# Performance work log

Hardware: AMD Instinct MI355X
Metric: run time of the kernel (lower is better)

Reference implementation:

```python
import jax, jax.numpy as jnp
import numpy as np

B, T, D = 2, 2048, 1024
H, DH, CTX = 16, 64, 2048
EPS = 1e-6

def setup_inputs() -> dict:
    key = jax.random.key(0)
    ks = jax.random.split(key, 8)
    s = lambda d: 1.0 / np.sqrt(d)
    return {
        'x':       jax.random.normal(ks[0], (B, T, D), jnp.float32),
        'w_norm1': jnp.ones((D,), jnp.float32),
        'w_qkv':   jax.random.normal(ks[1], (3 * D, D), jnp.float32) * s(D),
        'w_proj':  jax.random.normal(ks[2], (D, D), jnp.float32) * s(D),
        'w_norm2': jnp.ones((D,), jnp.float32),
        'w_gate':  jax.random.normal(ks[3], (4 * D, D), jnp.float32) * s(D),
        'w_up':    jax.random.normal(ks[4], (4 * D, D), jnp.float32) * s(D),
        'w_down':  jax.random.normal(ks[5], (D, 4 * D), jnp.float32) * s(4 * D),
        'step':    0,
    }

def _rmsnorm(x, w):
    return x * jax.lax.rsqrt(jnp.mean(x * x, axis=-1, keepdims=True) + EPS) * w

def reference(x, w_norm1, w_qkv, w_proj, w_norm2, w_gate, w_up, w_down, step):
    # Prefill path (kv_cache is None, step == 0): full causal attention over T tokens.
    b, t, d = x.shape
    scale = 1.0 / np.sqrt(DH)
    h = _rmsnorm(x, w_norm1)
    qkv = (h @ w_qkv.T).reshape(b, t, 3, H, DH).transpose(2, 0, 3, 1, 4)  # [3,B,H,T,Dh]
    q, k, v = qkv[0], qkv[1], qkv[2]
    att = jnp.einsum('bhqd,bhkd->bhqk', q, k) * scale           # [B,H,T,T]
    causal = jnp.tril(jnp.ones((t, t), bool))
    att = jnp.where(causal, att, jnp.float32(-jnp.inf))
    att = jax.nn.softmax(att, axis=-1)
    out = jnp.einsum('bhqk,bhkd->bhqd', att, v)                 # [B,H,T,Dh]
    out = out.transpose(0, 2, 1, 3).reshape(b, t, d)
    x = x + out @ w_proj.T
    h2 = _rmsnorm(x, w_norm2)
    x = x + (jax.nn.silu(h2 @ w_gate.T) * (h2 @ w_up.T)) @ w_down.T
    # Append-only KV cache, zero-padded to ctx length as in the torch module.
    k_cache = jnp.zeros((b, H, CTX, DH), x.dtype).at[:, :, :t].set(k)
    v_cache = jnp.zeros((b, H, CTX, DH), x.dtype).at[:, :, :t].set(v)
    return (x, k_cache, v_cache)
```

## Files before the change

### kernel.cpp

```cpp
#include <hip/hip_runtime.h>
#include <hip/hip_bf16.h>
#include <cstdint>
#include <cstddef>


using bf16x8 = __attribute__((ext_vector_type(8))) __bf16;
using f32x4  = __attribute__((ext_vector_type(4))) float;

#define VMCNT(n) asm volatile("s_waitcnt vmcnt(" #n ")" ::: "memory")
#define LGKM0()  do { asm volatile("s_waitcnt lgkmcnt(0)" ::: "memory"); \
                      __builtin_amdgcn_sched_barrier(0); } while (0)
#define BARF()   do { asm volatile("" ::: "memory"); __builtin_amdgcn_s_barrier(); \
                      asm volatile("" ::: "memory"); } while (0)

__device__ __forceinline__ short f2b(float f) {
  uint32_t u = __builtin_bit_cast(uint32_t, f);
  uint32_t r = (u + 0x7FFFu + ((u >> 16) & 1u)) >> 16;
  return (short)r;
}
__device__ __forceinline__ float b2f(short s) {
  uint32_t u = ((uint32_t)(uint16_t)s) << 16;
  return __builtin_bit_cast(float, u);
}
__device__ __forceinline__ uint32_t pack2(float a, float b) {
  return (__builtin_bit_cast(uint32_t, a) >> 16) |
         (__builtin_bit_cast(uint32_t, b) & 0xFFFF0000u);
}

__device__ __forceinline__ void gload16(const short* g, short* l) {
  __builtin_amdgcn_global_load_lds(
      (const __attribute__((address_space(1))) void*)g,
      (__attribute__((address_space(3))) void*)l, 16, 0, 0);
}

template<int ROWS>
__device__ __forceinline__ void stage_swz(const short* __restrict__ g, int ldg,
                                          short* lds, int tid) {
#pragma unroll
  for (int jj = 0; jj < ROWS / 32; ++jj) {
    int row = jj * 32 + (tid >> 3);
    int seg = tid & 7;
    gload16(g + (size_t)row * ldg + ((seg ^ (row & 7)) << 3),
            lds + row * 64 + (seg << 3));
  }
}

__device__ __forceinline__ void stage_round512(const short* __restrict__ g, int ldg,
                                               short* lds, int tid, int rbase) {
  int row = rbase + (tid >> 3);
  int seg = tid & 7;
  gload16(g + (size_t)row * ldg + ((seg ^ (row & 7)) << 3),
          lds + row * 64 + (seg << 3));
}

__device__ __forceinline__ bf16x8 frag64(const short* lds, int row, int seg) {
  return *(const bf16x8*)(lds + row * 64 + ((seg ^ (row & 7)) << 3));
}

__device__ __forceinline__ f32x4 mma16(bf16x8 a, bf16x8 b, f32x4 c) {
  return __builtin_amdgcn_mfma_f32_16x16x32_bf16(a, b, c, 0, 0, 0);
}

__global__ void k_cvt_all(const float* __restrict__ wqkv, short* __restrict__ oqkv,
                          const float* __restrict__ wproj, short* __restrict__ oproj,
                          const float* __restrict__ wgate, short* __restrict__ ogate,
                          const float* __restrict__ wup, short* __restrict__ oup,
                          const float* __restrict__ wdown, short* __restrict__ odown) {
  int bid = blockIdx.x;
  const float* src;
  short* dst;
  int off;
  if (bid < 3072)       { src = wqkv;  dst = oqkv;  off = bid; }
  else if (bid < 4096)  { src = wproj; dst = oproj; off = bid - 3072; }
  else if (bid < 8192)  { src = wgate; dst = ogate; off = bid - 4096; }
  else if (bid < 12288) { src = wup;   dst = oup;   off = bid - 8192; }
  else                  { src = wdown; dst = odown; off = bid - 12288; }
  int i = off * 256 + threadIdx.x;
  float4 v = ((const float4*)src)[i];
  ((short4*)dst)[i] = make_short4(f2b(v.x), f2b(v.y), f2b(v.z), f2b(v.w));
}

__global__ void k_rms(const float* __restrict__ x, const float* __restrict__ w,
                      short* __restrict__ out) {
  int row = blockIdx.x;
  int tid = threadIdx.x;
  float4 v = *(const float4*)(x + (size_t)row * 1024 + tid * 4);
  float ss = v.x * v.x + v.y * v.y + v.z * v.z + v.w * v.w;
#pragma unroll
  for (int o = 1; o < 64; o <<= 1) ss += __shfl_xor(ss, o);
  __shared__ float sred[4];
  int wid = tid >> 6, lane = tid & 63;
  if (lane == 0) sred[wid] = ss;
  __syncthreads();
  float tot = sred[0] + sred[1] + sred[2] + sred[3];
  float r = rsqrtf(tot * (1.0f / 1024.0f) + 1e-6f);
  float4 wv = *(const float4*)(w + tid * 4);
  short4 o = make_short4(f2b(v.x * r * wv.x), f2b(v.y * r * wv.y),
                         f2b(v.z * r * wv.z), f2b(v.w * r * wv.w));
  *(short4*)(out + (size_t)row * 1024 + tid * 4) = o;
}

__global__ __launch_bounds__(512) void k_qkv(
    const short* __restrict__ A, const short* __restrict__ W,
    short* __restrict__ q_b, short* __restrict__ k_b, short* __restrict__ vT_b,
    float* __restrict__ kc, float* __restrict__ vc) {
  const int K = 1024, nk = 16;
  __shared__ short As[2][128 * 64];
  __shared__ short Bq[2][128 * 64];
  __shared__ short Bk[2][128 * 64];
  __shared__ short Bv[2][128 * 64];
  int tid = threadIdx.x;
  int bid = blockIdx.x;
  int swz = (bid & 7) * 32 + (bid >> 3);
  int bx = swz & 7, by = swz >> 3;
  int m0 = by * 128, n0 = bx * 128;
  int w = tid >> 6, l = tid & 63;
  int wr = w >> 2, wc = w & 3;
  int lr = l & 15, lseg = l >> 4;
  f32x4 aq[4][2] = {}, ak[4][2] = {}, av[4][2] = {};
  const short* Ab = A + (size_t)m0 * K;
  const short* Qb = W + (size_t)n0 * K;
  const short* Kb = W + (size_t)(1024 + n0) * K;
  const short* Vb = W + (size_t)(2048 + n0) * K;

  stage_round512(Ab, K, &As[0][0], tid, 0);
  stage_round512(Ab, K, &As[0][0], tid, 64);
  stage_round512(Qb, K, &Bq[0][0], tid, 0);
  stage_round512(Qb, K, &Bq[0][0], tid, 64);
  stage_round512(Kb, K, &Bk[0][0], tid, 0);
  stage_round512(Kb, K, &Bk[0][0], tid, 64);
  stage_round512(Vb, K, &Bv[0][0], tid, 0);
  stage_round512(Vb, K, &Bv[0][0], tid, 64);
  stage_round512(Ab + 64, K, &As[1][0], tid, 0);
  stage_round512(Ab + 64, K, &As[1][0], tid, 64);

  bf16x8 a[4][2], b[2][2];
#pragma unroll 2
  for (int t = 0; t < nk; ++t) {
    short* Sa = &As[t & 1][0];
    short* Sq = &Bq[t & 1][0];
    short* Sk = &Bk[t & 1][0];
    short* Sv = &Bv[t & 1][0];
    short* SqN = &Bq[(t + 1) & 1][0];
    short* SkN = &Bk[(t + 1) & 1][0];
    short* SvN = &Bv[(t + 1) & 1][0];
    const short* Ag2 = Ab + (size_t)(t + 2) * 64;
    const short* Qg1 = Qb + (size_t)(t + 1) * 64;
    const short* Kg1 = Kb + (size_t)(t + 1) * 64;
    const short* Vg1 = Vb + (size_t)(t + 1) * 64;
    bool pf1 = (t + 1 < nk), pf2 = (t + 2 < nk);

    VMCNT(2);
    BARF();

#pragma unroll
    for (int i = 0; i < 4; ++i)
#pragma unroll
      for (int kk = 0; kk < 2; ++kk)
        a[i][kk] = frag64(Sa, wr * 64 + i * 16 + lr, kk * 4 + lseg);
#pragma unroll
    for (int j = 0; j < 2; ++j)
#pragma unroll
      for (int kk = 0; kk < 2; ++kk)
        b[j][kk] = frag64(Sq, wc * 32 + j * 16 + lr, kk * 4 + lseg);
    if (pf1) {
      stage_round512(Qg1, K, SqN, tid, 0);
      stage_round512(Qg1, K, SqN, tid, 64);
      stage_round512(Kg1, K, SkN, tid, 0);
      stage_round512(Kg1, K, SkN, tid, 64);
    }
    BARF();
    LGKM0();
    __builtin_amdgcn_s_setprio(1);
#pragma unroll
    for (int i = 0; i < 4; ++i)
#pragma unroll
      for (int j = 0; j < 2; ++j) {
        aq[i][j] = mma16(a[i][0], b[j][0], aq[i][j]);
        aq[i][j] = mma16(a[i][1], b[j][1], aq[i][j]);
      }
    __builtin_amdgcn_s_setprio(0);

#pragma unroll
    for (int j = 0; j < 2; ++j)
#pragma unroll
      for (int kk = 0; kk < 2; ++kk)
        b[j][kk] = frag64(Sk, wc * 32 + j * 16 + lr, kk * 4 + lseg);
    if (pf1) {
      stage_round512(Vg1, K, SvN, tid, 0);
      stage_round512(Vg1, K, SvN, tid, 64);
    }
    BARF();
    LGKM0();
    __builtin_amdgcn_s_setprio(1);
#pragma unroll
    for (int i = 0; i < 4; ++i)
#pragma unroll
      for (int j = 0; j < 2; ++j) {
        ak[i][j] = mma16(a[i][0], b[j][0], ak[i][j]);
        ak[i][j] = mma16(a[i][1], b[j][1], ak[i][j]);
      }
    __builtin_amdgcn_s_setprio(0);

#pragma unroll
    for (int j = 0; j < 2; ++j)
#pragma unroll
      for (int kk = 0; kk < 2; ++kk)
        b[j][kk] = frag64(Sv, wc * 32 + j * 16 + lr, kk * 4 + lseg);
    if (pf2) {
      stage_round512(Ag2, K, Sa, tid, 0);
      stage_round512(Ag2, K, Sa, tid, 64);
    }
    BARF();
    LGKM0();
    __builtin_amdgcn_s_setprio(1);
#pragma unroll
    for (int i = 0; i < 4; ++i)
#pragma unroll
      for (int j = 0; j < 2; ++j) {
        av[i][j] = mma16(a[i][0], b[j][0], av[i][j]);
        av[i][j] = mma16(a[i][1], b[j][1], av[i][j]);
      }
    __builtin_amdgcn_s_setprio(0);
  }

#pragma unroll
  for (int i = 0; i < 4; ++i) {
#pragma unroll
    for (int j = 0; j < 2; ++j) {
#pragma unroll
      for (int r = 0; r < 4; ++r) {
        int m = m0 + wr * 64 + i * 16 + lseg * 4 + r;
        int n = n0 + wc * 32 + j * 16 + lr;
        int hh = n >> 6, dh = n & 63;
        int b_ = m >> 11, tt = m & 2047;
        int bh = b_ * 16 + hh;
        size_t idx = ((size_t)bh * 2048 + tt) * 64 + dh;
        q_b[idx] = f2b(aq[i][j][r]);
        float fk = ak[i][j][r];
        k_b[idx] = f2b(fk);
        kc[idx] = fk;
        float fv = av[i][j][r];
        vT_b[((size_t)bh * 64 + dh) * 2048 + tt] = f2b(fv);
        vc[idx] = fv;
      }
    }
  }
}

__global__ __launch_bounds__(512) void k_mlp(
    const short* __restrict__ A, const short* __restrict__ Wg,
    const short* __restrict__ Wu, short* __restrict__ outb) {
  const int K = 1024, N = 4096, nk = 16;
  __shared__ short As[2][256 * 64];
  __shared__ short Bg[2][128 * 64];
  __shared__ short Bu[2][128 * 64];
  int tid = threadIdx.x;
  int nwg = gridDim.x, bid = blockIdx.x;
  int swz = (bid & 7) * (nwg >> 3) + (bid >> 3);
  int bx = swz & 31, by = swz >> 5;
  int m0 = by * 256, n0 = bx * 128;
  int w = tid >> 6, l = tid & 63;
  int wr = w >> 2, wc = w & 3;
  int lr = l & 15, lseg = l >> 4;
  f32x4 aG[2][4][2] = {}, aU[2][4][2] = {};
  const short* Ab = A + (size_t)m0 * K;
  const short* Gb = Wg + (size_t)n0 * K;
  const short* Ub = Wu + (size_t)n0 * K;

  stage_round512(Ab, K, &As[0][0], tid, 0);
  stage_round512(Ab, K, &As[0][0], tid, 64);
  stage_round512(Ab, K, &As[0][0], tid, 128);
  stage_round512(Ab, K, &As[0][0], tid, 192);
  stage_round512(Gb, K, &Bg[0][0], tid, 0);
  stage_round512(Gb, K, &Bg[0][0], tid, 64);
  stage_round512(Ub, K, &Bu[0][0], tid, 0);
  stage_round512(Ub, K, &Bu[0][0], tid, 64);
  stage_round512(Ab + 64, K, &As[1][0], tid, 0);
  stage_round512(Ab + 64, K, &As[1][0], tid, 64);
  stage_round512(Ab + 64, K, &As[1][0], tid, 128);
  stage_round512(Ab + 64, K, &As[1][0], tid, 192);

  bf16x8 a0[4][2], a1[4][2], bg[2][2], bu[2][2];
#pragma unroll 2
  for (int t = 0; t < nk; ++t) {
    short* Sa  = &As[t & 1][0];
    short* Sg  = &Bg[t & 1][0];
    short* Su  = &Bu[t & 1][0];
    short* SgN = &Bg[(t + 1) & 1][0];
    short* SuN = &Bu[(t + 1) & 1][0];
    const short* Ag2 = Ab + (size_t)(t + 2) * 64;
    const short* Gg1 = Gb + (size_t)(t + 1) * 64;
    const short* Ug1 = Ub + (size_t)(t + 1) * 64;
    bool pf1 = (t + 1 < nk), pf2 = (t + 2 < nk);

    VMCNT(4);
    BARF();

#pragma unroll
    for (int i = 0; i < 4; ++i)
#pragma unroll
      for (int kk = 0; kk < 2; ++kk)
        a0[i][kk] = frag64(Sa, wr * 128 + i * 16 + lr, kk * 4 + lseg);
#pragma unroll
    for (int j = 0; j < 2; ++j)
#pragma unroll
      for (int kk = 0; kk < 2; ++kk)
        bg[j][kk] = frag64(Sg, wc * 32 + j * 16 + lr, kk * 4 + lseg);
    if (pf1) {
      stage_round512(Gg1, K, SgN, tid, 0);
      stage_round512(Gg1, K, SgN, tid, 64);
      stage_round512(Ug1, K, SuN, tid, 0);
      stage_round512(Ug1, K, SuN, tid, 64);
    }
    BARF();
    LGKM0();
    __builtin_amdgcn_s_setprio(1);
#pragma unroll
    for (int i = 0; i < 4; ++i)
#pragma unroll
      for (int j = 0; j < 2; ++j) {
        aG[0][i][j] = mma16(a0[i][0], bg[j][0], aG[0][i][j]);
        aG[0][i][j] = mma16(a0[i][1], bg[j][1], aG[0][i][j]);
      }
    __builtin_amdgcn_s_setprio(0);

#pragma unroll
    for (int j = 0; j < 2; ++j)
#pragma unroll
      for (int kk = 0; kk < 2; ++kk)
        bu[j][kk] = frag64(Su, wc * 32 + j * 16 + lr, kk * 4 + lseg);
    if (pf2) {
      stage_round512(Ag2, K, Sa, tid, 0);
      stage_round512(Ag2, K, Sa, tid, 128);
    }
    BARF();
    LGKM0();
    __builtin_amdgcn_s_setprio(1);
#pragma unroll
    for (int i = 0; i < 4; ++i)
#pragma unroll
      for (int j = 0; j < 2; ++j) {
        aU[0][i][j] = mma16(a0[i][0], bu[j][0], aU[0][i][j]);
        aU[0][i][j] = mma16(a0[i][1], bu[j][1], aU[0][i][j]);
      }
    __builtin_amdgcn_s_setprio(0);

#pragma unroll
    for (int i = 0; i < 4; ++i)
#pragma unroll
      for (int kk = 0; kk < 2; ++kk)
        a1[i][kk] = frag64(Sa, wr * 128 + 64 + i * 16 + lr, kk * 4 + lseg);
    BARF();
    LGKM0();
    __builtin_amdgcn_s_setprio(1);
#pragma unroll
    for (int i = 0; i < 4; ++i)
#pragma unroll
      for (int j = 0; j < 2; ++j) {
        aG[1][i][j] = mma16(a1[i][0], bg[j][0], aG[1][i][j]);
        aG[1][i][j] = mma16(a1[i][1], bg[j][1], aG[1][i][j]);
      }
    __builtin_amdgcn_s_setprio(0);

    if (pf2) {
      stage_round512(Ag2, K, Sa, tid, 64);
      stage_round512(Ag2, K, Sa, tid, 192);
    }
    BARF();
    __builtin_amdgcn_s_setprio(1);
#pragma unroll
    for (int i = 0; i < 4; ++i)
#pragma unroll
      for (int j = 0; j < 2; ++j) {
        aU[1][i][j] = mma16(a1[i][0], bu[j][0], aU[1][i][j]);
        aU[1][i][j] = mma16(a1[i][1], bu[j][1], aU[1][i][j]);
      }
    __builtin_amdgcn_s_setprio(0);
  }

#pragma unroll
  for (int qm = 0; qm < 2; ++qm) {
#pragma unroll
    for (int i = 0; i < 4; ++i) {
#pragma unroll
      for (int j = 0; j < 2; ++j) {
#pragma unroll
        for (int r = 0; r < 4; ++r) {
          int m = m0 + wr * 128 + qm * 64 + i * 16 + (l >> 4) * 4 + r;
          int n = n0 + wc * 32 + j * 16 + lr;
          float g = aG[qm][i][j][r];
          float u = aU[qm][i][j][r];
          float s = g / (1.0f + __expf(-g));
          outb[(size_t)m * N + n] = f2b(s * u);
        }
      }
    }
  }
}

__global__ __launch_bounds__(256, 2) void k_gemm_skinny(
    const short* __restrict__ A, const short* __restrict__ Bw,
    int M, int N, int K, int gx,
    const float* __restrict__ res, float* __restrict__ outf) {
  __shared__ short As[3][128 * 64];
  __shared__ short Bs[3][64 * 64];
  int tid = threadIdx.x;
  int nwg = gridDim.x, bid = blockIdx.x;
  int swz = (bid & 7) * (nwg >> 3) + (bid >> 3);
  int bx = swz % gx, by = swz / gx;
  int m0 = by * 128, n0 = bx * 64;
  int w = tid >> 6, l = tid & 63;
  int wr = w >> 1, wc = w & 1;
  int lr = l & 15, lseg = l >> 4;
  f32x4 acc[4][2] = {};
  int nk = K >> 6;
  const short* Ab = A + (size_t)m0 * K;
  const short* Bb = Bw + (size_t)n0 * K;

  stage_swz<128>(Ab, K, &As[0][0], tid);
  stage_swz<64>(Bb, K, &Bs[0][0], tid);
  stage_swz<128>(Ab + 64, K, &As[1][0], tid);
  stage_swz<64>(Bb + 64, K, &Bs[1][0], tid);

#pragma unroll 1
  for (int u = 0; u < nk; ++u) {
    VMCNT(6);
    BARF();
    if (u + 2 < nk) {
      int sl = (u + 2) % 3;
      stage_swz<128>(Ab + (u + 2) * 64, K, &As[sl][0], tid);
      stage_swz<64>(Bb + (u + 2) * 64, K, &Bs[sl][0], tid);
    }
    const short* Asl = &As[u % 3][0];
    const short* Bsl = &Bs[u % 3][0];
    bf16x8 ar[4][2], br[2][2];
#pragma unroll
    for (int i = 0; i < 4; ++i)
#pragma unroll
      for (int kk = 0; kk < 2; ++kk)
        ar[i][kk] = frag64(Asl, wr * 64 + i * 16 + lr, kk * 4 + lseg);
#pragma unroll
    for (int j = 0; j < 2; ++j)
#pragma unroll
      for (int kk = 0; kk < 2; ++kk)
        br[j][kk] = frag64(Bsl, wc * 32 + j * 16 + lr, kk * 4 + lseg);
    LGKM0();
    __builtin_amdgcn_s_setprio(1);
#pragma unroll
    for (int i = 0; i < 4; ++i)
#pragma unroll
      for (int j = 0; j < 2; ++j) {
        acc[i][j] = mma16(ar[i][0], br[j][0], acc[i][j]);
        acc[i][j] = mma16(ar[i][1], br[j][1], acc[i][j]);
      }
    __builtin_amdgcn_s_setprio(0);
  }

#pragma unroll
  for (int i = 0; i < 4; ++i) {
#pragma unroll
    for (int j = 0; j < 2; ++j) {
#pragma unroll
      for (int r = 0; r < 4; ++r) {
        int m = m0 + wr * 64 + i * 16 + (l >> 4) * 4 + r;
        int n = n0 + wc * 32 + j * 16 + lr;
        outf[(size_t)m * N + n] = acc[i][j][r] + res[(size_t)m * N + n];
      }
    }
  }
}

template<int NC>
__device__ __forceinline__ void attn_tile(
    const short* __restrict__ Ksl, const short* __restrict__ Vsl,
    short* __restrict__ pw,
    const bf16x8 (&qf)[2][2], f32x4 (&acc)[2][4],
    float (&mrow)[2], float (&dden)[2],
    int kv0, int qb0, int qb1, bool band0, bool band1,
    int lr, int g) {
  bf16x8 kf[4][2], vb[2][4];
#pragma unroll
  for (int i = 0; i < 4; ++i)
#pragma unroll
    for (int kk = 0; kk < 2; ++kk)
      kf[i][kk] = frag64(Ksl, i * 16 + lr, kk * 4 + g);
#pragma unroll
  for (int kk = 0; kk < 2; ++kk)
#pragma unroll
    for (int jf = 0; jf < 4; ++jf)
      vb[kk][jf] = frag64(Vsl, jf * 16 + lr, kk * 4 + g);

  f32x4 st[NC][4];
#pragma unroll
  for (int c = 0; c < NC; ++c) {
    int cc = (NC == 2) ? c : 1;
#pragma unroll
    for (int i = 0; i < 4; ++i) {
      f32x4 z = {};
      z = mma16(kf[i][0], qf[cc][0], z);
      z = mma16(kf[i][1], qf[cc][1], z);
      st[c][i] = z;
    }
  }

  const float SC = 0.125f * 1.44269504f;
  float p[NC][16], pm[NC], corr[NC];
#pragma unroll
  for (int c = 0; c < NC; ++c) {
    int cc = (NC == 2) ? c : 1;
    bool band = (cc == 0) ? band0 : band1;
    int qgc = ((cc == 0) ? qb0 : qb1) + lr;
    float m_ = -INFINITY;
#pragma unroll
    for (int i = 0; i < 4; ++i)
#pragma unroll
      for (int r = 0; r < 4; ++r) {
        float v = st[c][i][r] * SC;
        if (band) {
          int key = kv0 + i * 16 + g * 4 + r;
          if (key > qgc) v = -INFINITY;
        }
        p[c][i * 4 + r] = v;
        m_ = fmaxf(m_, v);
      }
    pm[c] = m_;
  }
#pragma unroll
  for (int c = 0; c < NC; ++c) pm[c] = fmaxf(pm[c], __shfl_xor(pm[c], 16));
#pragma unroll
  for (int c = 0; c < NC; ++c) pm[c] = fmaxf(pm[c], __shfl_xor(pm[c], 32));
  float dsum[NC];
#pragma unroll
  for (int c = 0; c < NC; ++c) {
    int cc = (NC == 2) ? c : 1;
    float nm = fmaxf(mrow[cc], pm[c]);
    corr[c] = exp2f(mrow[cc] - nm);
    mrow[cc] = nm;
    float ds_ = 0.0f;
#pragma unroll
    for (int kx = 0; kx < 16; ++kx) {
      float pv = exp2f(p[c][kx] - nm);
      p[c][kx] = pv;
      ds_ += pv;
    }
    dsum[c] = ds_;
  }
#pragma unroll
  for (int c = 0; c < NC; ++c) dsum[c] += __shfl_xor(dsum[c], 16);
#pragma unroll
  for (int c = 0; c < NC; ++c) dsum[c] += __shfl_xor(dsum[c], 32);
#pragma unroll
  for (int c = 0; c < NC; ++c) {
    int cc = (NC == 2) ? c : 1;
    dden[cc] = dden[cc] * corr[c] + dsum[c];
  }

#pragma unroll
  for (int c = 0; c < NC; ++c) {
    int cc = (NC == 2) ? c : 1;
#pragma unroll
    for (int r = 0; r < 4; ++r) {
      float cr = __shfl(corr[c], g * 4 + r);
#pragma unroll
      for (int jf = 0; jf < 4; ++jf) acc[cc][jf][r] *= cr;
    }
    int prow = cc * 16 + lr;
#pragma unroll
    for (int i = 0; i < 4; ++i) {
      uint2 pk;
      pk.x = pack2(p[c][i * 4 + 0], p[c][i * 4 + 1]);
      pk.y = pack2(p[c][i * 4 + 2], p[c][i * 4 + 3]);
      int seg = (i * 2 + (g >> 1)) ^ (prow & 7);
      *(uint2*)(pw + prow * 64 + seg * 8 + (g & 1) * 4) = pk;
    }
  }

#pragma unroll
  for (int c = 0; c < NC; ++c) {
    int cc = (NC == 2) ? c : 1;
    int prow = cc * 16 + lr;
#pragma unroll
    for (int kk = 0; kk < 2; ++kk) {
      bf16x8 pa = *(const bf16x8*)(pw + prow * 64 + (((kk * 4 + g) ^ (prow & 7)) << 3));
#pragma unroll
      for (int jf = 0; jf < 4; ++jf)
        acc[cc][jf] = mma16(pa, vb[kk][jf], acc[cc][jf]);
    }
  }
}

__global__ __launch_bounds__(256, 2) void k_attn(const short* __restrict__ q_b,
                                                 const short* __restrict__ k_b,
                                                 const short* __restrict__ vT_b,
                                                 short* __restrict__ o_b) {
  __shared__ short Ks[3][64 * 64];
  __shared__ short VTs[3][64 * 64];
  __shared__ short Ps[4][32 * 64];
  int tid = threadIdx.x;
  int w = tid >> 6, l = tid & 63;
  int lr = l & 15, g = l >> 4;
  int ib = blockIdx.x, bh = blockIdx.y;
  int qlo = ib, qhi = 31 - ib;
  int qb0 = qlo * 64 + w * 16;
  int qb1 = qhi * 64 + w * 16;

  bf16x8 qf[2][2];
  const short* Qg = q_b + (size_t)bh * 2048 * 64;
#pragma unroll
  for (int kk = 0; kk < 2; ++kk) {
    qf[0][kk] = *(const bf16x8*)(Qg + (size_t)(qb0 + lr) * 64 + kk * 32 + g * 8);
    qf[1][kk] = *(const bf16x8*)(Qg + (size_t)(qb1 + lr) * 64 + kk * 32 + g * 8);
  }

  f32x4 acc[2][4] = {};
  float mrow[2] = {-INFINITY, -INFINITY};
  float dden[2] = {0.0f, 0.0f};
  int nt = qhi + 1;
  const short* Kg = k_b + (size_t)bh * 2048 * 64;
  const short* Vg = vT_b + (size_t)bh * 64 * 2048;
  short* pw = &Ps[w][0];

  stage_swz<64>(Kg, 64, &Ks[0][0], tid);
  stage_swz<64>(Vg, 2048, &VTs[0][0], tid);
  stage_swz<64>(Kg + 64 * 64, 64, &Ks[1][0], tid);
  stage_swz<64>(Vg + 64, 2048, &VTs[1][0], tid);

#pragma unroll 1
  for (int kt = 0; kt <= qlo; ++kt) {
    VMCNT(4);
    BARF();
    if (kt + 2 < nt) {
      int sl = (kt + 2) % 3;
      stage_swz<64>(Kg + (size_t)(kt + 2) * 64 * 64, 64, &Ks[sl][0], tid);
      stage_swz<64>(Vg + (kt + 2) * 64, 2048, &VTs[sl][0], tid);
    }
    int s = kt % 3;
    attn_tile<2>(&Ks[s][0], &VTs[s][0], pw, qf, acc, mrow, dden,
                 kt * 64, qb0, qb1, kt == qlo, false, lr, g);
  }
#pragma unroll 1
  for (int kt = qlo + 1; kt < nt; ++kt) {
    VMCNT(4);
    BARF();
    if (kt + 2 < nt) {
      int sl = (kt + 2) % 3;
      stage_swz<64>(Kg + (size_t)(kt + 2) * 64 * 64, 64, &Ks[sl][0], tid);
      stage_swz<64>(Vg + (kt + 2) * 64, 2048, &VTs[sl][0], tid);
    }
    int s = kt % 3;
    attn_tile<1>(&Ks[s][0], &VTs[s][0], pw, qf, acc, mrow, dden,
                 kt * 64, qb0, qb1, false, kt == qhi, lr, g);
  }

  int hh = bh & 15, b_ = bh >> 4;
#pragma unroll
  for (int c = 0; c < 2; ++c) {
    int qbc = (c == 0) ? qb0 : qb1;
#pragma unroll
    for (int r = 0; r < 4; ++r) {
      float dq = __shfl(dden[c], g * 4 + r);
      float inv = 1.0f / dq;
      int mg = qbc + g * 4 + r;
      size_t rowoff = ((size_t)b_ * 2048 + mg) * 1024 + hh * 64;
#pragma unroll
      for (int jf = 0; jf < 4; ++jf)
        o_b[rowoff + jf * 16 + lr] = f2b(acc[c][jf][r] * inv);
    }
  }
}

extern "C" void kernel_launch(void* const* d_in, const int* in_sizes, int n_in,
                              void* d_out, int out_size, void* d_ws, size_t ws_size,
                              hipStream_t stream) {
  const float* x     = (const float*)d_in[0];
  const float* wn1   = (const float*)d_in[1];
  const float* wqkv  = (const float*)d_in[2];
  const float* wproj = (const float*)d_in[3];
  const float* wn2   = (const float*)d_in[4];
  const float* wgate = (const float*)d_in[5];
  const float* wup   = (const float*)d_in[6];
  const float* wdown = (const float*)d_in[7];
  float* out = (float*)d_out;
  char* ws = (char*)d_ws;

  short* wqkv_b  = (short*)(ws + 0);
  short* wproj_b = (short*)(ws + 6291456);
  short* wgate_b = (short*)(ws + 8388608);
  short* wup_b   = (short*)(ws + 16777216);
  short* wdown_b = (short*)(ws + 25165824);
  short* h_b     = (short*)(ws + 33554432);
  short* q_b     = (short*)(ws + 41943040);
  short* k_b     = (short*)(ws + 50331648);
  short* vT_b    = (short*)(ws + 58720256);
  short* ao_b    = (short*)(ws + 67108864);
  short* act_b   = q_b;
  float* x1 = out;
  float* kc = out + 4194304;
  float* vc = out + 8388608;

  k_cvt_all<<<16384, 256, 0, stream>>>(wqkv, wqkv_b, wproj, wproj_b,
                                       wgate, wgate_b, wup, wup_b, wdown, wdown_b);

  k_rms<<<4096, 256, 0, stream>>>(x, wn1, h_b);

  k_qkv<<<256, 512, 0, stream>>>(h_b, wqkv_b, q_b, k_b, vT_b, kc, vc);

  k_attn<<<dim3(16, 32), 256, 0, stream>>>(q_b, k_b, vT_b, ao_b);

  k_gemm_skinny<<<512, 256, 0, stream>>>(ao_b, wproj_b, 4096, 1024, 1024, 16,
                                         x, x1);

  k_rms<<<4096, 256, 0, stream>>>(x1, wn2, h_b);

  k_mlp<<<512, 512, 0, stream>>>(h_b, wgate_b, wup_b, act_b);

  k_gemm_skinny<<<512, 256, 0, stream>>>(act_b, wdown_b, 4096, 1024, 4096, 16,
                                         x1, out);
}
```

Before: 279.6 us.

## Halve GEMM grids to one wave of workgroups with larger per-block tiles

The MLP gate/up kernel now launches 256 workgroups, and each one loops over two adjacent 128-column output tiles, restaging the A tile for each half. The skinny GEMM used for the projection and down projection grows its M tile from 128 to 256 rows, doubles the accumulators and drops from a three-stage to a two-stage buffer with a full vmcnt wait. The aim is a single full wave of blocks on the 256 CUs to avoid a tail wave, plus more reuse of each B tile. In exchange there is less latency hiding (vmcnt 0, double buffering), more register and LDS pressure, and the MLP's two halves run serially inside each block.

```diff
diff --git a/kernel.cpp b/kernel.cpp
--- a/kernel.cpp
+++ b/kernel.cpp
@@ -256,146 +256,152 @@
   __shared__ short Bg[2][128 * 64];
   __shared__ short Bu[2][128 * 64];
   int tid = threadIdx.x;
-  int nwg = gridDim.x, bid = blockIdx.x;
-  int swz = (bid & 7) * (nwg >> 3) + (bid >> 3);
-  int bx = swz & 31, by = swz >> 5;
-  int m0 = by * 256, n0 = bx * 128;
+  int bid = blockIdx.x;
+  int swz = (bid & 7) * 32 + (bid >> 3);
+  int bxp = swz & 15, by = swz >> 4;
+  int m0 = by * 256;
   int w = tid >> 6, l = tid & 63;
   int wr = w >> 2, wc = w & 3;
   int lr = l & 15, lseg = l >> 4;
-  f32x4 aG[2][4][2] = {}, aU[2][4][2] = {};
   const short* Ab = A + (size_t)m0 * K;
-  const short* Gb = Wg + (size_t)n0 * K;
-  const short* Ub = Wu + (size_t)n0 * K;
-
-  stage_round512(Ab, K, &As[0][0], tid, 0);
-  stage_round512(Ab, K, &As[0][0], tid, 64);
-  stage_round512(Ab, K, &As[0][0], tid, 128);
-  stage_round512(Ab, K, &As[0][0], tid, 192);
-  stage_round512(Gb, K, &Bg[0][0], tid, 0);
-  stage_round512(Gb, K, &Bg[0][0], tid, 64);
-  stage_round512(Ub, K, &Bu[0][0], tid, 0);
-  stage_round512(Ub, K, &Bu[0][0], tid, 64);
-  stage_round512(Ab + 64, K, &As[1][0], tid, 0);
-  stage_round512(Ab + 64, K, &As[1][0], tid, 64);
-  stage_round512(Ab + 64, K, &As[1][0], tid, 128);
-  stage_round512(Ab + 64, K, &As[1][0], tid, 192);
-
-  bf16x8 a0[4][2], a1[4][2], bg[2][2], bu[2][2];
+
+#pragma unroll 1
+  for (int hf = 0; hf < 2; ++hf) {
+    int n0 = (bxp * 2 + hf) * 128;
+    const short* Gb = Wg + (size_t)n0 * K;
+    const short* Ub = Wu + (size_t)n0 * K;
+    f32x4 aG[2][4][2] = {}, aU[2][4][2] = {};
+
+    stage_round512(Ab, K, &As[0][0], tid, 0);
+    stage_round512(Ab, K, &As[0][0], tid, 64);
+    stage_round512(Ab, K, &As[0][0], tid, 128);
+    stage_round512(Ab, K, &As[0][0], tid, 192);
+    stage_round512(Gb, K, &Bg[0][0], tid, 0);
+    stage_round512(Gb, K, &Bg[0][0], tid, 64);
+    stage_round512(Ub, K, &Bu[0][0], tid, 0);
+    stage_round512(Ub, K, &Bu[0][0], tid, 64);
+    stage_round512(Ab + 64, K, &As[1][0], tid, 0);
+    stage_round512(Ab + 64, K, &As[1][0], tid, 64);
+    stage_round512(Ab + 64, K, &As[1][0], tid, 128);
+    stage_round512(Ab + 64, K, &As[1][0], tid, 192);
+
+    bf16x8 a0[4][2], a1[4][2], bg[2][2], bu[2][2];
 #pragma unroll 2
-  for (int t = 0; t < nk; ++t) {
-    short* Sa  = &As[t & 1][0];
-    short* Sg  = &Bg[t & 1][0];
-    short* Su  = &Bu[t & 1][0];
-    short* SgN = &Bg[(t + 1) & 1][0];
-    short* SuN = &Bu[(t + 1) & 1][0];
-    const short* Ag2 = Ab + (size_t)(t + 2) * 64;
-    const short* Gg1 = Gb + (size_t)(t + 1) * 64;
-    const short* Ug1 = Ub + (size_t)(t + 1) * 64;
-    bool pf1 = (t + 1 < nk), pf2 = (t + 2 < nk);
-
-    VMCNT(4);
+    for (int t = 0; t < nk; ++t) {
+      short* Sa  = &As[t & 1][0];
+      short* Sg  = &Bg[t & 1][0];
+      short* Su  = &Bu[t & 1][0];
+      short* SgN = &Bg[(t + 1) & 1][0];
+      short* SuN = &Bu[(t + 1) & 1][0];
+      const short* Ag2 = Ab + (size_t)(t + 2) * 64;
+      const short* Gg1 = Gb + (size_t)(t + 1) * 64;
+      const short* Ug1 = Ub + (size_t)(t + 1) * 64;
+      bool pf1 = (t + 1 < nk), pf2 = (t + 2 < nk);
+
+      VMCNT(4);
+      BARF();
+
+#pragma unroll
+      for (int i = 0; i < 4; ++i)
+#pragma unroll
+        for (int kk = 0; kk < 2; ++kk)
+          a0[i][kk] = frag64(Sa, wr * 128 + i * 16 + lr, kk * 4 + lseg);
+#pragma unroll
+      for (int j = 0; j < 2; ++j)
+#pragma unroll
+        for (int kk = 0; kk < 2; ++kk)
+          bg[j][kk] = frag64(Sg, wc * 32 + j * 16 + lr, kk * 4 + lseg);
+      if (pf1) {
+        stage_round512(Gg1, K, SgN, tid, 0);
+        stage_round512(Gg1, K, SgN, tid, 64);
+        stage_round512(Ug1, K, SuN, tid, 0);
+        stage_round512(Ug1, K, SuN, tid, 64);
+      }
+      BARF();
+      LGKM0();
+      __builtin_amdgcn_s_setprio(1);
+#pragma unroll
+      for (int i = 0; i < 4; ++i)
+#pragma unroll
+        for (int j = 0; j < 2; ++j) {
+          aG[0][i][j] = mma16(a0[i][0], bg[j][0], aG[0][i][j]);
+          aG[0][i][j] = mma16(a0[i][1], bg[j][1], aG[0][i][j]);
+        }
+      __builtin_amdgcn_s_setprio(0);
+
+#pragma unroll
+      for (int j = 0; j < 2; ++j)
+#pragma unroll
+        for (int kk = 0; kk < 2; ++kk)
+          bu[j][kk] = frag64(Su, wc * 32 + j * 16 + lr, kk * 4 + lseg);
+      if (pf2) {
+        stage_round512(Ag2, K, Sa, tid, 0);
+        stage_round512(Ag2, K, Sa, tid, 128);
+      }
+      BARF();
+      LGKM0();
+      __builtin_amdgcn_s_setprio(1);
+#pragma unroll
+      for (int i = 0; i < 4; ++i)
+#pragma unroll
+        for (int j = 0; j < 2; ++j) {
+          aU[0][i][j] = mma16(a0[i][0], bu[j][0], aU[0][i][j]);
+          aU[0][i][j] = mma16(a0[i][1], bu[j][1], aU[0][i][j]);
+        }
+      __builtin_amdgcn_s_setprio(0);
+
+#pragma unroll
+      for (int i = 0; i < 4; ++i)
+#pragma unroll
+        for (int kk = 0; kk < 2; ++kk)
+          a1[i][kk] = frag64(Sa, wr * 128 + 64 + i * 16 + lr, kk * 4 + lseg);
+      BARF();
+      LGKM0();
+      __builtin_amdgcn_s_setprio(1);
+#pragma unroll
+      for (int i = 0; i < 4; ++i)
+#pragma unroll
+        for (int j = 0; j < 2; ++j) {
+          aG[1][i][j] = mma16(a1[i][0], bg[j][0], aG[1][i][j]);
+          aG[1][i][j] = mma16(a1[i][1], bg[j][1], aG[1][i][j]);
+        }
+      __builtin_amdgcn_s_setprio(0);
+
+      if (pf2) {
+        stage_round512(Ag2, K, Sa, tid, 64);
+        stage_round512(Ag2, K, Sa, tid, 192);
+      }
+      BARF();
+      __builtin_amdgcn_s_setprio(1);
+#pragma unroll
+      for (int i = 0; i < 4; ++i)
+#pragma unroll
+        for (int j = 0; j < 2; ++j) {
+          aU[1][i][j] = mma16(a1[i][0], bu[j][0], aU[1][i][j]);
+          aU[1][i][j] = mma16(a1[i][1], bu[j][1], aU[1][i][j]);
+        }
+      __builtin_amdgcn_s_setprio(0);
+    }
+
+#pragma unroll
+    for (int qm = 0; qm < 2; ++qm) {
+#pragma unroll
+      for (int i = 0; i < 4; ++i) {
+#pragma unroll
+        for (int j = 0; j < 2; ++j) {
+#pragma unroll
+          for (int r = 0; r < 4; ++r) {
+            int m = m0 + wr * 128 + qm * 64 + i * 16 + lseg * 4 + r;
+            int n = n0 + wc * 32 + j * 16 + lr;
+            float g = aG[qm][i][j][r];
+            float u = aU[qm][i][j][r];
+            float s = g / (1.0f + __expf(-g));
+            outb[(size_t)m * N + n] = f2b(s * u);
+          }
+        }
+      }
+    }
     BARF();
-
-#pragma unroll
-    for (int i = 0; i < 4; ++i)
-#pragma unroll
-      for (int kk = 0; kk < 2; ++kk)
-        a0[i][kk] = frag64(Sa, wr * 128 + i * 16 + lr, kk * 4 + lseg);
-#pragma unroll
-    for (int j = 0; j < 2; ++j)
-#pragma unroll
-      for (int kk = 0; kk < 2; ++kk)
-        bg[j][kk] = frag64(Sg, wc * 32 + j * 16 + lr, kk * 4 + lseg);
-    if (pf1) {
-      stage_round512(Gg1, K, SgN, tid, 0);
-      stage_round512(Gg1, K, SgN, tid, 64);
-      stage_round512(Ug1, K, SuN, tid, 0);
-      stage_round512(Ug1, K, SuN, tid, 64);
-    }
-    BARF();
-    LGKM0();
-    __builtin_amdgcn_s_setprio(1);
-#pragma unroll
-    for (int i = 0; i < 4; ++i)
-#pragma unroll
-      for (int j = 0; j < 2; ++j) {
-        aG[0][i][j] = mma16(a0[i][0], bg[j][0], aG[0][i][j]);
-        aG[0][i][j] = mma16(a0[i][1], bg[j][1], aG[0][i][j]);
-      }
-    __builtin_amdgcn_s_setprio(0);
-
-#pragma unroll
-    for (int j = 0; j < 2; ++j)
-#pragma unroll
-      for (int kk = 0; kk < 2; ++kk)
-        bu[j][kk] = frag64(Su, wc * 32 + j * 16 + lr, kk * 4 + lseg);
-    if (pf2) {
-      stage_round512(Ag2, K, Sa, tid, 0);
-      stage_round512(Ag2, K, Sa, tid, 128);
-    }
-    BARF();
-    LGKM0();
-    __builtin_amdgcn_s_setprio(1);
-#pragma unroll
-    for (int i = 0; i < 4; ++i)
-#pragma unroll
-      for (int j = 0; j < 2; ++j) {
-        aU[0][i][j] = mma16(a0[i][0], bu[j][0], aU[0][i][j]);
-        aU[0][i][j] = mma16(a0[i][1], bu[j][1], aU[0][i][j]);
-      }
-    __builtin_amdgcn_s_setprio(0);
-
-#pragma unroll
-    for (int i = 0; i < 4; ++i)
-#pragma unroll
-      for (int kk = 0; kk < 2; ++kk)
-        a1[i][kk] = frag64(Sa, wr * 128 + 64 + i * 16 + lr, kk * 4 + lseg);
-    BARF();
-    LGKM0();
-    __builtin_amdgcn_s_setprio(1);
-#pragma unroll
-    for (int i = 0; i < 4; ++i)
-#pragma unroll
-      for (int j = 0; j < 2; ++j) {
-        aG[1][i][j] = mma16(a1[i][0], bg[j][0], aG[1][i][j]);
-        aG[1][i][j] = mma16(a1[i][1], bg[j][1], aG[1][i][j]);
-      }
-    __builtin_amdgcn_s_setprio(0);
-
-    if (pf2) {
-      stage_round512(Ag2, K, Sa, tid, 64);
-      stage_round512(Ag2, K, Sa, tid, 192);
-    }
-    BARF();
-    __builtin_amdgcn_s_setprio(1);
-#pragma unroll
-    for (int i = 0; i < 4; ++i)
-#pragma unroll
-      for (int j = 0; j < 2; ++j) {
-        aU[1][i][j] = mma16(a1[i][0], bu[j][0], aU[1][i][j]);
-        aU[1][i][j] = mma16(a1[i][1], bu[j][1], aU[1][i][j]);
-      }
-    __builtin_amdgcn_s_setprio(0);
-  }
-
-#pragma unroll
-  for (int qm = 0; qm < 2; ++qm) {
-#pragma unroll
-    for (int i = 0; i < 4; ++i) {
-#pragma unroll
-      for (int j = 0; j < 2; ++j) {
-#pragma unroll
-        for (int r = 0; r < 4; ++r) {
-          int m = m0 + wr * 128 + qm * 64 + i * 16 + (l >> 4) * 4 + r;
-          int n = n0 + wc * 32 + j * 16 + lr;
-          float g = aG[qm][i][j][r];
-          float u = aU[qm][i][j][r];
-          float s = g / (1.0f + __expf(-g));
-          outb[(size_t)m * N + n] = f2b(s * u);
-        }
-      }
-    }
   }
 }
 
@@ -403,67 +409,80 @@
     const short* __restrict__ A, const short* __restrict__ Bw,
     int M, int N, int K, int gx,
     const float* __restrict__ res, float* __restrict__ outf) {
-  __shared__ short As[3][128 * 64];
-  __shared__ short Bs[3][64 * 64];
+  __shared__ short As[2][256 * 64];
+  __shared__ short Bs[2][64 * 64];
   int tid = threadIdx.x;
   int nwg = gridDim.x, bid = blockIdx.x;
   int swz = (bid & 7) * (nwg >> 3) + (bid >> 3);
   int bx = swz % gx, by = swz / gx;
-  int m0 = by * 128, n0 = bx * 64;
+  int m0 = by * 256, n0 = bx * 64;
   int w = tid >> 6, l = tid & 63;
   int wr = w >> 1, wc = w & 1;
   int lr = l & 15, lseg = l >> 4;
-  f32x4 acc[4][2] = {};
+  f32x4 acc[8][2] = {};
   int nk = K >> 6;
   const short* Ab = A + (size_t)m0 * K;
   const short* Bb = Bw + (size_t)n0 * K;
 
-  stage_swz<128>(Ab, K, &As[0][0], tid);
+  stage_swz<256>(Ab, K, &As[0][0], tid);
   stage_swz<64>(Bb, K, &Bs[0][0], tid);
-  stage_swz<128>(Ab + 64, K, &As[1][0], tid);
-  stage_swz<64>(Bb + 64, K, &Bs[1][0], tid);
-
+
+  bf16x8 a[4][2], b[2][2];
 #pragma unroll 1
   for (int u = 0; u < nk; ++u) {
-    VMCNT(6);
+    int s = u & 1;
+    VMCNT(0);
     BARF();
-    if (u + 2 < nk) {
-      int sl = (u + 2) % 3;
-      stage_swz<128>(Ab + (u + 2) * 64, K, &As[sl][0], tid);
-      stage_swz<64>(Bb + (u + 2) * 64, K, &Bs[sl][0], tid);
-    }
-    const short* Asl = &As[u % 3][0];
-    const short* Bsl = &Bs[u % 3][0];
-    bf16x8 ar[4][2], br[2][2];
+    if (u + 1 < nk) {
+      stage_swz<256>(Ab + (u + 1) * 64, K, &As[s ^ 1][0], tid);
+      stage_swz<64>(Bb + (u + 1) * 64, K, &Bs[s ^ 1][0], tid);
+    }
+    const short* Asl = &As[s][0];
+    const short* Bsl = &Bs[s][0];
 #pragma unroll
     for (int i = 0; i < 4; ++i)
 #pragma unroll
       for (int kk = 0; kk < 2; ++kk)
-        ar[i][kk] = frag64(Asl, wr * 64 + i * 16 + lr, kk * 4 + lseg);
+        a[i][kk] = frag64(Asl, wr * 128 + i * 16 + lr, kk * 4 + lseg);
 #pragma unroll
     for (int j = 0; j < 2; ++j)
 #pragma unroll
       for (int kk = 0; kk < 2; ++kk)
-        br[j][kk] = frag64(Bsl, wc * 32 + j * 16 + lr, kk * 4 + lseg);
+        b[j][kk] = frag64(Bsl, wc * 32 + j * 16 + lr, kk * 4 + lseg);
     LGKM0();
     __builtin_amdgcn_s_setprio(1);
 #pragma unroll
     for (int i = 0; i < 4; ++i)
 #pragma unroll
       for (int j = 0; j < 2; ++j) {
-        acc[i][j] = mma16(ar[i][0], br[j][0], acc[i][j]);
-        acc[i][j] = mma16(ar[i][1], br[j][1], acc[i][j]);
+        acc[i][j] = mma16(a[i][0], b[j][0], acc[i][j]);
+        acc[i][j] = mma16(a[i][1], b[j][1], acc[i][j]);
       }
     __builtin_amdgcn_s_setprio(0);
-  }
-
-#pragma unroll
-  for (int i = 0; i < 4; ++i) {
+#pragma unroll
+    for (int i = 0; i < 4; ++i)
+#pragma unroll
+      for (int kk = 0; kk < 2; ++kk)
+        a[i][kk] = frag64(Asl, wr * 128 + 64 + i * 16 + lr, kk * 4 + lseg);
+    LGKM0();
+    __builtin_amdgcn_s_setprio(1);
+#pragma unroll
+    for (int i = 0; i < 4; ++i)
+#pragma unroll
+      for (int j = 0; j < 2; ++j) {
+        acc[4 + i][j] = mma16(a[i][0], b[j][0], acc[4 + i][j]);
+        acc[4 + i][j] = mma16(a[i][1], b[j][1], acc[4 + i][j]);
+      }
+    __builtin_amdgcn_s_setprio(0);
+  }
+
+#pragma unroll
+  for (int i = 0; i < 8; ++i) {
 #pragma unroll
     for (int j = 0; j < 2; ++j) {
 #pragma unroll
       for (int r = 0; r < 4; ++r) {
-        int m = m0 + wr * 64 + i * 16 + (l >> 4) * 4 + r;
+        int m = m0 + wr * 128 + i * 16 + lseg * 4 + r;
         int n = n0 + wc * 32 + j * 16 + lr;
         outf[(size_t)m * N + n] = acc[i][j][r] + res[(size_t)m * N + n];
       }
@@ -708,13 +727,13 @@
 
   k_attn<<<dim3(16, 32), 256, 0, stream>>>(q_b, k_b, vT_b, ao_b);
 
-  k_gemm_skinny<<<512, 256, 0, stream>>>(ao_b, wproj_b, 4096, 1024, 1024, 16,
+  k_gemm_skinny<<<256, 256, 0, stream>>>(ao_b, wproj_b, 4096, 1024, 1024, 16,
                                          x, x1);
 
   k_rms<<<4096, 256, 0, stream>>>(x1, wn2, h_b);
 
-  k_mlp<<<512, 512, 0, stream>>>(h_b, wgate_b, wup_b, act_b);
-
-  k_gemm_skinny<<<512, 256, 0, stream>>>(act_b, wdown_b, 4096, 1024, 4096, 16,
+  k_mlp<<<256, 512, 0, stream>>>(h_b, wgate_b, wup_b, act_b);
+
+  k_gemm_skinny<<<256, 256, 0, stream>>>(act_b, wdown_b, 4096, 1024, 4096, 16,
                                          x1, out);
 }
```

New measurement: 318.7 us. 1.14x slower.
